# Kernel optimization log

Hardware: AMD Instinct MI355X
Metric: run time of the kernel (lower is better)

The kernel has to match this reference:

```python
import jax, jax.numpy as jnp
import numpy as np

B, S, H, V, T, NS, NB, NSW = 16, 200, 400, 25000, 8, 30, 3, 36


def setup_inputs() -> dict:
    key = jax.random.key(0)
    ks = jax.random.split(key, 12)
    return {
        "encoded_hidden": jax.random.normal(ks[0], (1, B, H), jnp.float32),
        "encoded_outputs": jax.random.normal(ks[1], (B, S, H), jnp.float32),
        "story": jax.random.randint(ks[2], (B, S), 0, V),
        "target_batches": jax.random.randint(ks[3], (B, NS, T), 0, V),
        "slot_dom_idx": jax.random.randint(ks[4], (NS,), 0, NSW),
        "slot_slot_idx": jax.random.randint(ks[5], (NS,), 0, NSW),
        "emb_W": jax.random.normal(ks[6], (V, H), jnp.float32) * 0.05,
        "slot_emb_W": jax.random.normal(ks[7], (NSW, H), jnp.float32) * 0.1,
        "gru_W_ih": jax.random.normal(ks[8], (3 * H, H), jnp.float32) * 0.05,
        "gru_W_hh": jax.random.normal(ks[9], (3 * H, H), jnp.float32) * 0.05,
        "gru_b_ih": jnp.zeros((3 * H,), jnp.float32),
        "gru_b_hh": jnp.zeros((3 * H,), jnp.float32),
        "W_ratio_w": jax.random.normal(ks[10], (1, 3 * H), jnp.float32) * 0.05,
        "W_ratio_b": jnp.zeros((1,), jnp.float32),
        "W_gate_w": jax.random.normal(ks[11], (NB, H), jnp.float32) * 0.05,
        "W_gate_b": jnp.zeros((NB,), jnp.float32),
    }


def reference(encoded_hidden, encoded_outputs, story, target_batches,
              slot_dom_idx, slot_slot_idx, emb_W, slot_emb_W,
              gru_W_ih, gru_W_hh, gru_b_ih, gru_b_hh,
              W_ratio_w, W_ratio_b, W_gate_w, W_gate_b):
    b, s, h = encoded_outputs.shape
    ns = slot_dom_idx.shape[0]
    v = emb_W.shape[0]
    t = target_batches.shape[2]
    bs = ns * b  # flattened slot*batch dim (parallel decode over slots)

    # slot embedding = domain_emb + slot_emb, broadcast over batch
    slot_emb = slot_emb_W[slot_dom_idx] + slot_emb_W[slot_slot_idx]        # [ns,h]
    dec_in0 = jnp.broadcast_to(slot_emb[:, None, :], (ns, b, h)).reshape(bs, h)
    h0 = jnp.tile(encoded_hidden[0], (ns, 1))                              # [bs,h]
    enc = jnp.tile(encoded_outputs, (ns, 1, 1))                            # [bs,s,h]
    pad_mask = jnp.tile(story == 0, (ns, 1))                               # [bs,s]
    story_rep = jnp.tile(story, (ns, 1))                                   # [bs,s]
    # teacher forcing targets, slot-major flatten: [bs, t]
    tf = jnp.transpose(target_batches, (1, 0, 2)).reshape(bs, t)
    rows = jnp.arange(bs)

    def gru_cell(x, hid):
        gx = x @ gru_W_ih.T + gru_b_ih
        gh = hid @ gru_W_hh.T + gru_b_hh
        r = jax.nn.sigmoid(gx[:, :h] + gh[:, :h])
        z = jax.nn.sigmoid(gx[:, h:2 * h] + gh[:, h:2 * h])
        n = jnp.tanh(gx[:, 2 * h:] + r * gh[:, 2 * h:])
        return (1.0 - z) * n + z * hid

    def step(carry, tgt_t):
        hid, x = carry
        hid = gru_cell(x, hid)                                             # [bs,h]
        scores = jnp.einsum('bh,bsh->bs', hid, enc)
        scores = jnp.where(pad_mask, -jnp.inf, scores)
        prob = jax.nn.softmax(scores, axis=1)                              # [bs,s]
        ctx = jnp.einsum('bs,bsh->bh', prob, enc)                          # [bs,h]
        p_vocab = jax.nn.softmax(hid @ emb_W.T, axis=1)                    # [bs,v]
        switch = jax.nn.sigmoid(
            jnp.concatenate([hid, ctx, x], axis=-1) @ W_ratio_w.T + W_ratio_b)  # [bs,1]
        p_ctx = jnp.zeros((bs, v), p_vocab.dtype).at[rows[:, None], story_rep].add(prob)
        final = (1.0 - switch) * p_ctx + switch * p_vocab                  # [bs,v]
        x_next = emb_W[tgt_t]                                              # teacher forcing
        return (hid, x_next), (final, ctx)

    (_, _), (finals, ctxs) = jax.lax.scan(step, (h0, dec_in0), tf.T)
    all_point = jnp.transpose(finals.reshape(t, ns, b, v), (1, 2, 0, 3))   # [ns,b,t,v]
    all_gate = (ctxs[0] @ W_gate_w.T + W_gate_b).reshape(ns, b, -1)        # [ns,b,nb_gate]
    return all_point, all_gate
```

## Files before the change

### kernel.cpp

```cpp
#include <hip/hip_runtime.h>
#include <math.h>

#define B_   16
#define S_   200
#define H_   400
#define V_   25000
#define T_   8
#define NS_  30
#define NB_  3
#define NSW_ 36
#define BS_  480

#define KP_  448
#define MP_  512
#define NP_  25088
#define NG_  1280
#define MA_  3840
#define NVT_ (NP_/128)
#define PSL_ 200

typedef unsigned short u16;
typedef __attribute__((ext_vector_type(4))) float f32x4;
typedef __attribute__((ext_vector_type(8))) short short8;

__device__ __forceinline__ u16 f2bf(float f) {
    unsigned u = __float_as_uint(f);
    u += 0x7FFFu + ((u >> 16) & 1u);
    return (u16)(u >> 16);
}
__device__ __forceinline__ float bf2f(u16 v) {
    return __uint_as_float(((unsigned)v) << 16);
}
__device__ __forceinline__ float wred_sum(float v) {
    v += __shfl_xor(v, 32); v += __shfl_xor(v, 16); v += __shfl_xor(v, 8);
    v += __shfl_xor(v, 4);  v += __shfl_xor(v, 2);  v += __shfl_xor(v, 1);
    return v;
}
__device__ __forceinline__ float wred_max(float v) {
    v = fmaxf(v, __shfl_xor(v, 32)); v = fmaxf(v, __shfl_xor(v, 16));
    v = fmaxf(v, __shfl_xor(v, 8));  v = fmaxf(v, __shfl_xor(v, 4));
    v = fmaxf(v, __shfl_xor(v, 2));  v = fmaxf(v, __shfl_xor(v, 1));
    return v;
}

__device__ __forceinline__ void gload_lds16(const void* g, void* l) {
    __builtin_amdgcn_global_load_lds(
        (const __attribute__((address_space(1))) void*)g,
        (__attribute__((address_space(3))) void*)l, 16, 0, 0);
}

#define MFMA_SETUP()                                                          \
    const int wid = tid >> 6, lane = tid & 63;                                \
    const int wr = wid >> 1, wc = wid & 1;                                    \
    f32x4 acc[4][4] = {};                                                     \
    const int sslot = lane & 7;                                               \
    const int srow8 = (lane >> 3) & 7;                                        \
    const int lcol = (sslot ^ srow8) * 8;                                     \
    const int lr = lane & 15, lg = lane >> 4, lx = lane & 7;                  \
    const int sA0 = (lg ^ lx) * 8, sA1 = ((4 + lg) ^ lx) * 8;

#define STAGE_TILE(k0_)                                                       \
    {                                                                         \
        _Pragma("unroll")                                                     \
        for (int is = 0; is < 4; ++is) {                                      \
            gload_lds16(Ag + (size_t)is * 8 * KP_ + (k0_),                    \
                        &As[(wid * 32 + is * 8) * 64]);                       \
            gload_lds16(Bg + (size_t)is * 8 * KP_ + (k0_),                    \
                        &Bs[(wid * 32 + is * 8) * 64]);                       \
        }                                                                     \
    }

#define COMPUTE_TILE()                                                        \
    {                                                                         \
        short8 af[4][2], bfr[4][2];                                           \
        _Pragma("unroll")                                                     \
        for (int i = 0; i < 4; ++i) {                                         \
            int ra = (wr * 64 + i * 16 + lr) * 64;                            \
            af[i][0] = *reinterpret_cast<const short8*>(&As[ra + sA0]);       \
            af[i][1] = *reinterpret_cast<const short8*>(&As[ra + sA1]);       \
            int rb = (wc * 64 + i * 16 + lr) * 64;                            \
            bfr[i][0] = *reinterpret_cast<const short8*>(&Bs[rb + sA0]);      \
            bfr[i][1] = *reinterpret_cast<const short8*>(&Bs[rb + sA1]);      \
        }                                                                     \
        _Pragma("unroll")                                                     \
        for (int h = 0; h < 2; ++h)                                           \
            _Pragma("unroll")                                                 \
            for (int i = 0; i < 4; ++i)                                       \
                _Pragma("unroll")                                             \
                for (int j = 0; j < 4; ++j)                                   \
                    acc[i][j] = __builtin_amdgcn_mfma_f32_16x16x32_bf16(      \
                        af[i][h], bfr[j][h], acc[i][j], 0, 0, 0);             \
    }

#define MFMA_KLOOP_SB()                                                       \
    _Pragma("unroll")                                                         \
    for (int kt = 0; kt < 7; ++kt) {                                          \
        STAGE_TILE(kt * 64);                                                  \
        __syncthreads();                                                      \
        COMPUTE_TILE();                                                       \
        __syncthreads();                                                      \
    }

__global__ void init_all(const float* __restrict__ eh, float* __restrict__ hid,
                         u16* __restrict__ Ab) {
    int i = blockIdx.x * blockDim.x + threadIdx.x;
    if (i >= MP_ * KP_) return;
    int row = i / KP_, d = i - row * KP_;
    u16 v = 0;
    if (row < BS_ && d < H_) {
        float h = eh[(row % B_) * H_ + d];
        hid[row * H_ + d] = h;
        v = f2bf(h);
    }
    Ab[i] = v;
}

__device__ __forceinline__ void conv_chunk(const float* __restrict__ src,
                                           u16* __restrict__ dst, int i, int rows) {
    int row = i / (KP_ / 8), c8 = (i - row * (KP_ / 8)) * 8;
    short8 o = {};
    if (row < rows && c8 < H_) {
        const float4* s = reinterpret_cast<const float4*>(src + (size_t)row * H_ + c8);
        float4 a = s[0], b = s[1];
        o[0] = (short)f2bf(a.x); o[1] = (short)f2bf(a.y);
        o[2] = (short)f2bf(a.z); o[3] = (short)f2bf(a.w);
        o[4] = (short)f2bf(b.x); o[5] = (short)f2bf(b.y);
        o[6] = (short)f2bf(b.z); o[7] = (short)f2bf(b.w);
    }
    *reinterpret_cast<short8*>(dst + (size_t)row * KP_ + c8) = o;
}

__global__ void conv_all(const float* __restrict__ embW, const float* __restrict__ Wih,
                         const float* __restrict__ Whh, u16* __restrict__ Bb,
                         u16* __restrict__ Wihb, u16* __restrict__ Whhb) {
    const int CB = NP_ * (KP_ / 8), CG = NG_ * (KP_ / 8);
    int i = blockIdx.x * blockDim.x + threadIdx.x;
    if (i < CB) conv_chunk(embW, Bb, i, V_);
    else if (i < CB + CG) conv_chunk(Wih, Wihb, i - CB, 3 * H_);
    else if (i < CB + 2 * CG) conv_chunk(Whh, Whhb, i - CB - CG, 3 * H_);
}

__global__ void xall_prep(const int* __restrict__ tb, const float* __restrict__ embW,
                          const float* __restrict__ sembW,
                          const int* __restrict__ dom, const int* __restrict__ sli,
                          float* __restrict__ x_all, u16* __restrict__ Xb_all) {
    int i = blockIdx.x * blockDim.x + threadIdx.x;
    if (i >= MA_ * (KP_ / 8)) return;
    int row = i / (KP_ / 8), c8 = (i - row * (KP_ / 8)) * 8;
    int t = row / BS_, r = row - t * BS_;
    int batch = r % B_, slot = r / B_;
    short8 o = {};
    if (c8 < H_) {
        float4 a, b;
        if (t == 0) {
            const float4* s0 = reinterpret_cast<const float4*>(sembW + dom[slot] * H_ + c8);
            const float4* s1 = reinterpret_cast<const float4*>(sembW + sli[slot] * H_ + c8);
            float4 x0 = s0[0], x1 = s0[1], y0 = s1[0], y1 = s1[1];
            a = make_float4(x0.x + y0.x, x0.y + y0.y, x0.z + y0.z, x0.w + y0.w);
            b = make_float4(x1.x + y1.x, x1.y + y1.y, x1.z + y1.z, x1.w + y1.w);
        } else {
            int tok = tb[(batch * NS_ + slot) * T_ + (t - 1)];
            const float4* s = reinterpret_cast<const float4*>(embW + (size_t)tok * H_ + c8);
            a = s[0]; b = s[1];
        }
        o[0] = (short)f2bf(a.x); o[1] = (short)f2bf(a.y);
        o[2] = (short)f2bf(a.z); o[3] = (short)f2bf(a.w);
        o[4] = (short)f2bf(b.x); o[5] = (short)f2bf(b.y);
        o[6] = (short)f2bf(b.z); o[7] = (short)f2bf(b.w);
        *reinterpret_cast<float4*>(x_all + (size_t)row * H_ + c8) = a;
        *reinterpret_cast<float4*>(x_all + (size_t)row * H_ + c8 + 4) = b;
    }
    *reinterpret_cast<short8*>(Xb_all + (size_t)row * KP_ + c8) = o;
}

__global__ __launch_bounds__(256)
void gemm_setup(const u16* __restrict__ Xb_all, const u16* __restrict__ Abuf,
                const u16* __restrict__ Wihb, const u16* __restrict__ Whhb,
                float* __restrict__ gx_all, float* __restrict__ gh) {
    __shared__ u16 As[128 * 64];
    __shared__ u16 Bs[128 * 64];
    const int tid = threadIdx.x;
    const bool mainp = blockIdx.y < (MA_ / 128);
    const int m0 = (mainp ? blockIdx.y : blockIdx.y - MA_ / 128) * 128;
    const int n0 = blockIdx.x * 128;
    const u16* A = mainp ? Xb_all : Abuf;
    const u16* Bw = mainp ? Wihb : Whhb;
    float* C = mainp ? gx_all : gh;
    const int Mlim = mainp ? MA_ : BS_;

    MFMA_SETUP();
    const u16* Ag = A + (size_t)(m0 + wid * 32 + (lane >> 3)) * KP_ + lcol;
    const u16* Bg = Bw + (size_t)(n0 + wid * 32 + (lane >> 3)) * KP_ + lcol;
    MFMA_KLOOP_SB();

    const int m_base = m0 + wr * 64 + lg * 4;
    const int n_base = n0 + wc * 64 + lr;
    #pragma unroll
    for (int i = 0; i < 4; ++i)
        #pragma unroll
        for (int r = 0; r < 4; ++r) {
            int m = m_base + i * 16 + r;
            if (m >= Mlim) continue;
            #pragma unroll
            for (int j = 0; j < 4; ++j) {
                int n = n_base + j * 16;
                if (n < 3 * H_) C[(size_t)m * 3 * H_ + n] = acc[i][j][r];
            }
        }
}

__global__ __launch_bounds__(256, 2)
void vocab_gh(const u16* __restrict__ A, const u16* __restrict__ Bb,
              const u16* __restrict__ Whhb, u16* __restrict__ pb,
              float* __restrict__ psum, float* __restrict__ gh) {
    __shared__ u16 As[256 * 64];
    __shared__ u16 Bs[128 * 64];
    __shared__ float sred[2][256];
    const int bid = blockIdx.x;
    const int tid = threadIdx.x;
    const int xcd = bid & 7, idx = bid >> 3;
    const int lin = (xcd < 4) ? (xcd * 52 + idx) : (208 + (xcd - 4) * 51 + idx);
    const int ntall = lin >> 1, mt = lin & 1;
    const bool isv = (ntall < NVT_);
    const int n0 = (isv ? ntall : ntall - NVT_) * 128;
    const int m0 = mt * 256;
    const u16* Bsrc = isv ? Bb : Whhb;

    const int wid = tid >> 6, lane = tid & 63;
    const int wr = wid >> 1, wc = wid & 1;
    f32x4 acc[8][4] = {};
    const int sslot = lane & 7;
    const int srow8 = (lane >> 3) & 7;
    const int lcol = (sslot ^ srow8) * 8;
    const int lr = lane & 15, lg = lane >> 4, lx = lane & 7;
    const int sA0 = (lg ^ lx) * 8, sA1 = ((4 + lg) ^ lx) * 8;

    const u16* Ag = A + (size_t)(m0 + wid * 64 + (lane >> 3)) * KP_ + lcol;
    const u16* Bg = Bsrc + (size_t)(n0 + wid * 32 + (lane >> 3)) * KP_ + lcol;

    for (int kt = 0; kt < 7; ++kt) {
        const int k0 = kt * 64;
        #pragma unroll
        for (int is = 0; is < 8; ++is)
            gload_lds16(Ag + (size_t)is * 8 * KP_ + k0, &As[(wid * 64 + is * 8) * 64]);
        #pragma unroll
        for (int is = 0; is < 4; ++is)
            gload_lds16(Bg + (size_t)is * 8 * KP_ + k0, &Bs[(wid * 32 + is * 8) * 64]);
        __syncthreads();
        #pragma unroll
        for (int h = 0; h < 2; ++h) {
            const int sA = h ? sA1 : sA0;
            short8 af[8], bf[4];
            #pragma unroll
            for (int i = 0; i < 8; ++i)
                af[i] = *reinterpret_cast<const short8*>(&As[(wr * 128 + i * 16 + lr) * 64 + sA]);
            #pragma unroll
            for (int j = 0; j < 4; ++j)
                bf[j] = *reinterpret_cast<const short8*>(&Bs[(wc * 64 + j * 16 + lr) * 64 + sA]);
            #pragma unroll
            for (int i = 0; i < 8; ++i)
                #pragma unroll
                for (int j = 0; j < 4; ++j)
                    acc[i][j] = __builtin_amdgcn_mfma_f32_16x16x32_bf16(
                        af[i], bf[j], acc[i][j], 0, 0, 0);
        }
        __syncthreads();
    }

    const int m_base = m0 + wr * 128 + lg * 4;
    const int n_base = n0 + wc * 64 + lr;
    if (isv) {
        #pragma unroll
        for (int i = 0; i < 8; ++i) {
            #pragma unroll
            for (int r = 0; r < 4; ++r) {
                int m = m_base + i * 16 + r;
                float js = 0.f;
                #pragma unroll
                for (int j = 0; j < 4; ++j) {
                    int n = n_base + j * 16;
                    float e = __expf(acc[i][j][r]);
                    if (m < BS_ && n < V_) {
                        pb[(size_t)m * V_ + n] = f2bf(e);
                        js += e;
                    }
                }
                js += __shfl_xor(js, 1);
                js += __shfl_xor(js, 2);
                js += __shfl_xor(js, 4);
                js += __shfl_xor(js, 8);
                if ((lane & 15) == 0) sred[wc][m - m0] = js;
            }
        }
        __syncthreads();
        {
            int m = m0 + tid;
            psum[(size_t)m * PSL_ + ntall] = sred[0][tid] + sred[1][tid];
        }
    } else {
        #pragma unroll
        for (int i = 0; i < 8; ++i)
            #pragma unroll
            for (int r = 0; r < 4; ++r) {
                int m = m_base + i * 16 + r;
                if (m >= BS_) continue;
                #pragma unroll
                for (int j = 0; j < 4; ++j) {
                    int n = n_base + j * 16;
                    if (n < 3 * H_) gh[(size_t)m * 3 * H_ + n] = acc[i][j][r];
                }
            }
    }
}

__global__ __launch_bounds__(256)
void attn_fin(const float* __restrict__ gx_all, const float* __restrict__ gh,
              const float* __restrict__ bih, const float* __restrict__ bhh,
              float* __restrict__ hid, u16* __restrict__ Ab,
              const float* __restrict__ x_all,
              const float* __restrict__ enc, const int* __restrict__ story,
              const float* __restrict__ Wr, const float* __restrict__ Wrb,
              const float* __restrict__ Wg, const float* __restrict__ Wgb,
              float* __restrict__ prob_cur, float* __restrict__ sw_cur,
              float* __restrict__ gate_out,
              float* __restrict__ out, const u16* __restrict__ pb,
              const float* __restrict__ psum, const float* __restrict__ sw_prev,
              const float* __restrict__ prob_prev, int t) {
    const int bid = blockIdx.x;
    const int lin = (bid & 7) * 120 + (bid >> 3);
    const int work = lin >> 1, kind = lin & 1;
    const int tid = threadIdx.x, w = tid >> 6, l = tid & 63;
    __shared__ __align__(16) float hs[H_];
    __shared__ __align__(16) float xs[H_];
    __shared__ __align__(16) float cs[H_];
    __shared__ float sc[S_];
    __shared__ float red[16];

    if (kind == 1) {
        if (t == 0) return;
        const int row = work, batch = row % B_;
        float rs = (tid < NVT_) ? psum[(size_t)row * PSL_ + tid] : 0.f;
        rs = wred_sum(rs);
        if (l == 0) red[w] = rs;
        __syncthreads();
        float denom = red[0] + red[1] + red[2] + red[3];
        float swv = sw_prev[row];
        float scl = swv / denom;
        const u16* ps = pb + (size_t)row * V_;
        float* p = out + ((size_t)row * T_ + (t - 1)) * V_;
        for (int v = tid * 8; v < V_; v += 256 * 8) {
            short8 in = *reinterpret_cast<const short8*>(ps + v);
            float4 o0, o1;
            o0.x = bf2f((u16)in[0]) * scl; o0.y = bf2f((u16)in[1]) * scl;
            o0.z = bf2f((u16)in[2]) * scl; o0.w = bf2f((u16)in[3]) * scl;
            o1.x = bf2f((u16)in[4]) * scl; o1.y = bf2f((u16)in[5]) * scl;
            o1.z = bf2f((u16)in[6]) * scl; o1.w = bf2f((u16)in[7]) * scl;
            *reinterpret_cast<float4*>(p + v) = o0;
            *reinterpret_cast<float4*>(p + v + 4) = o1;
        }
        __syncthreads();
        float om = 1.f - swv;
        for (int s = tid; s < S_; s += 256) {
            int tok = story[batch * S_ + s];
            atomicAdd(p + tok, om * prob_prev[(size_t)row * S_ + s]);
        }
        return;
    }

    const int batch = work / 30, slot = work - batch * 30;
    const int row = slot * B_ + batch;

    const float* gxr = gx_all + ((size_t)t * BS_ + row) * 3 * H_;
    const float* ghr = gh + (size_t)row * 3 * H_;
    const float* xr  = x_all + ((size_t)t * BS_ + row) * H_;
    for (int d = tid; d < H_; d += 256) {
        float r = 1.f / (1.f + expf(-(gxr[d] + bih[d] + ghr[d] + bhh[d])));
        float z = 1.f / (1.f + expf(-(gxr[H_ + d] + bih[H_ + d] + ghr[H_ + d] + bhh[H_ + d])));
        float n = tanhf(gxr[2 * H_ + d] + bih[2 * H_ + d] + r * (ghr[2 * H_ + d] + bhh[2 * H_ + d]));
        float h = (1.f - z) * n + z * hid[(size_t)row * H_ + d];
        hs[d] = h;
        hid[(size_t)row * H_ + d] = h;
        Ab[(size_t)row * KP_ + d] = f2bf(h);
        xs[d] = xr[d];
    }
    __syncthreads();

    const float* encb = enc + (size_t)batch * S_ * H_;
    {
        float4 hv1 = *reinterpret_cast<const float4*>(&hs[l * 4]);
        float4 hv2 = make_float4(0.f, 0.f, 0.f, 0.f);
        if (l < 36) hv2 = *reinterpret_cast<const float4*>(&hs[256 + l * 4]);
        for (int k = 0; k < 50; ++k) {
            int s = w * 50 + k;
            const float4* e = reinterpret_cast<const float4*>(encb + (size_t)s * H_);
            float4 ev = e[l];
            float part = ev.x * hv1.x + ev.y * hv1.y + ev.z * hv1.z + ev.w * hv1.w;
            if (l < 36) {
                float4 ev2 = e[64 + l];
                part += ev2.x * hv2.x + ev2.y * hv2.y + ev2.z * hv2.z + ev2.w * hv2.w;
            }
            part = wred_sum(part);
            if (l == 0)
                sc[s] = (story[batch * S_ + s] == 0) ? -1e30f : part;
        }
    }
    __syncthreads();

    float v = (tid < S_) ? sc[tid] : -1e30f;
    float wm = wred_max(v);
    if (l == 0) red[w] = wm;
    __syncthreads();
    float mx = fmaxf(fmaxf(red[0], red[1]), fmaxf(red[2], red[3]));
    float e = (tid < S_) ? __expf(v - mx) : 0.f;
    float wsum = wred_sum(e);
    if (l == 0) red[4 + w] = wsum;
    __syncthreads();
    float inv = 1.f / (red[4] + red[5] + red[6] + red[7]);
    if (tid < S_) {
        float pv = e * inv;
        sc[tid] = pv;
        prob_cur[(size_t)row * S_ + tid] = pv;
    }
    __syncthreads();

    for (int d = tid; d < H_; d += 256) {
        float a0 = 0.f, a1 = 0.f;
        for (int s = 0; s < S_; s += 2) {
            a0 += sc[s] * encb[(size_t)s * H_ + d];
            a1 += sc[s + 1] * encb[(size_t)(s + 1) * H_ + d];
        }
        cs[d] = a0 + a1;
    }
    __syncthreads();

    float part = 0.f;
    for (int i = tid; i < 3 * H_; i += 256) {
        float xv = (i < H_) ? hs[i] : (i < 2 * H_) ? cs[i - H_] : xs[i - 2 * H_];
        part += xv * Wr[i];
    }
    part = wred_sum(part);
    if (l == 0) red[8 + w] = part;
    __syncthreads();
    if (tid == 0)
        sw_cur[row] = 1.f / (1.f + expf(-(red[8] + red[9] + red[10] + red[11] + Wrb[0])));

    if (t == 0 && tid < NB_) {
        float acc = 0.f;
        for (int d = 0; d < H_; ++d) acc += cs[d] * Wg[tid * H_ + d];
        gate_out[(size_t)row * NB_ + tid] = acc + Wgb[tid];
    }
}

__global__ __launch_bounds__(256)
void scale_scatter(float* __restrict__ out, const u16* __restrict__ pb,
                   const float* __restrict__ psum, const float* __restrict__ sw,
                   const float* __restrict__ prob, const int* __restrict__ story) {
    const int row = blockIdx.x;
    const int tid = threadIdx.x, w = tid >> 6, l = tid & 63;
    __shared__ float red[4];
    float rs = (tid < NVT_) ? psum[(size_t)row * PSL_ + tid] : 0.f;
    rs = wred_sum(rs);
    if (l == 0) red[w] = rs;
    __syncthreads();
    float denom = red[0] + red[1] + red[2] + red[3];
    float swv = sw[row];
    float scl = swv / denom;
    const u16* ps = pb + (size_t)row * V_;
    float* p = out + ((size_t)row * T_ + (T_ - 1)) * V_;
    for (int v = tid * 8; v < V_; v += 256 * 8) {
        short8 in = *reinterpret_cast<const short8*>(ps + v);
        float4 o0, o1;
        o0.x = bf2f((u16)in[0]) * scl; o0.y = bf2f((u16)in[1]) * scl;
        o0.z = bf2f((u16)in[2]) * scl; o0.w = bf2f((u16)in[3]) * scl;
        o1.x = bf2f((u16)in[4]) * scl; o1.y = bf2f((u16)in[5]) * scl;
        o1.z = bf2f((u16)in[6]) * scl; o1.w = bf2f((u16)in[7]) * scl;
        *reinterpret_cast<float4*>(p + v) = o0;
        *reinterpret_cast<float4*>(p + v + 4) = o1;
    }
    __syncthreads();
    const int batch = row % B_;
    float om = 1.f - swv;
    for (int s = tid; s < S_; s += 256) {
        int tok = story[batch * S_ + s];
        atomicAdd(p + tok, om * prob[(size_t)row * S_ + s]);
    }
}

extern "C" void kernel_launch(void* const* d_in, const int* in_sizes, int n_in,
                              void* d_out, int out_size, void* d_ws, size_t ws_size,
                              hipStream_t stream) {
    const float* eh    = (const float*)d_in[0];
    const float* enc   = (const float*)d_in[1];
    const int*   story = (const int*)d_in[2];
    const int*   tb    = (const int*)d_in[3];
    const int*   dom   = (const int*)d_in[4];
    const int*   sli   = (const int*)d_in[5];
    const float* embW  = (const float*)d_in[6];
    const float* sembW = (const float*)d_in[7];
    const float* Wih   = (const float*)d_in[8];
    const float* Whh   = (const float*)d_in[9];
    const float* bih   = (const float*)d_in[10];
    const float* bhh   = (const float*)d_in[11];
    const float* Wr    = (const float*)d_in[12];
    const float* Wrb   = (const float*)d_in[13];
    const float* Wg    = (const float*)d_in[14];
    const float* Wgb   = (const float*)d_in[15];

    float* out = (float*)d_out;
    float* ws  = (float*)d_ws;

    float* gx_all = ws;
    float* gh     = gx_all + (size_t)MA_ * 3 * H_;
    float* hid    = gh + (size_t)BS_ * 3 * H_;
    float* x_all  = hid + (size_t)BS_ * H_;
    float* prob2  = x_all + (size_t)MA_ * H_;
    float* sw2    = prob2 + 2 * BS_ * S_;
    float* psum   = sw2 + 2 * BS_;
    u16* Ab     = (u16*)(psum + (size_t)MP_ * PSL_);
    u16* Xb_all = Ab + (size_t)MP_ * KP_;
    u16* Wihb   = Xb_all + (size_t)MA_ * KP_;
    u16* Whhb   = Wihb + (size_t)NG_ * KP_;
    u16* Bb     = Whhb + (size_t)NG_ * KP_;
    u16* pb     = Bb + (size_t)NP_ * KP_;
    size_t need = (size_t)((char*)(pb + (size_t)BS_ * V_) - (char*)ws);
    if (ws_size < need) return;

    float* gate_out = out + (size_t)NS_ * B_ * T_ * V_;

    init_all<<<(MP_ * KP_ + 255) / 256, 256, 0, stream>>>(eh, hid, Ab);
    {
        int tot = (NP_ + 2 * NG_) * (KP_ / 8);
        conv_all<<<(tot + 255) / 256, 256, 0, stream>>>(embW, Wih, Whh, Bb, Wihb, Whhb);
    }
    xall_prep<<<(MA_ * (KP_ / 8) + 255) / 256, 256, 0, stream>>>(tb, embW, sembW, dom, sli,
                                                                 x_all, Xb_all);
    gemm_setup<<<dim3(NG_ / 128, MA_ / 128 + MP_ / 128), 256, 0, stream>>>(
        Xb_all, Ab, Wihb, Whhb, gx_all, gh);

    for (int t = 0; t < T_; ++t) {
        const int cur = t & 1, prev = cur ^ 1;
        attn_fin<<<960, 256, 0, stream>>>(gx_all, gh, bih, bhh, hid, Ab, x_all,
                                          enc, story, Wr, Wrb, Wg, Wgb,
                                          prob2 + cur * BS_ * S_, sw2 + cur * BS_,
                                          gate_out, out, pb, psum,
                                          sw2 + prev * BS_, prob2 + prev * BS_ * S_, t);
        vocab_gh<<<412, 256, 0, stream>>>(Ab, Bb, Whhb, pb, psum, gh);
    }
    {
        const int last = (T_ - 1) & 1;
        scale_scatter<<<BS_, 256, 0, stream>>>(out, pb, psum, sw2 + last * BS_,
                                               prob2 + last * BS_ * S_, story);
    }
}
```

Baseline: 777.9 us.

## Double-buffer B tiles in vocab GEMM and merge prep kernels into one launch

The vocab_gh K-loop now double-buffers the B (weight) tile in shared memory. It prefetches the next K-slice while computing the current one, uses an explicit vmcnt wait instead of waiting for all loads, and replaces __syncthreads with raw s_barrier. The three setup kernels (init, weight conversion, x_all prep) are fused into one prep_all launch to save launch overhead. The gemm_setup macros are inlined with no functional change. The risks are extra LDS use, which may lower occupancy, and the hand-written waitcnt count, which must match the number of outstanding loads exactly or the kernel will read incomplete data.

```diff
diff --git a/kernel.cpp b/kernel.cpp
--- a/kernel.cpp
+++ b/kernel.cpp
@@ -8,7 +8,6 @@
 #define T_   8
 #define NS_  30
 #define NB_  3
-#define NSW_ 36
 #define BS_  480
 
 #define KP_  448
@@ -42,7 +41,6 @@
     v = fmaxf(v, __shfl_xor(v, 2));  v = fmaxf(v, __shfl_xor(v, 1));
     return v;
 }
-
 __device__ __forceinline__ void gload_lds16(const void* g, void* l) {
     __builtin_amdgcn_global_load_lds(
         (const __attribute__((address_space(1))) void*)g,
@@ -53,124 +51,76 @@
     const int wid = tid >> 6, lane = tid & 63;                                \
     const int wr = wid >> 1, wc = wid & 1;                                    \
     f32x4 acc[4][4] = {};                                                     \
-    const int sslot = lane & 7;                                               \
-    const int srow8 = (lane >> 3) & 7;                                        \
-    const int lcol = (sslot ^ srow8) * 8;                                     \
+    const int lcol = ((lane & 7) ^ ((lane >> 3) & 7)) * 8;                    \
     const int lr = lane & 15, lg = lane >> 4, lx = lane & 7;                  \
     const int sA0 = (lg ^ lx) * 8, sA1 = ((4 + lg) ^ lx) * 8;
 
-#define STAGE_TILE(k0_)                                                       \
-    {                                                                         \
-        _Pragma("unroll")                                                     \
-        for (int is = 0; is < 4; ++is) {                                      \
-            gload_lds16(Ag + (size_t)is * 8 * KP_ + (k0_),                    \
-                        &As[(wid * 32 + is * 8) * 64]);                       \
-            gload_lds16(Bg + (size_t)is * 8 * KP_ + (k0_),                    \
-                        &Bs[(wid * 32 + is * 8) * 64]);                       \
-        }                                                                     \
-    }
-
-#define COMPUTE_TILE()                                                        \
-    {                                                                         \
-        short8 af[4][2], bfr[4][2];                                           \
-        _Pragma("unroll")                                                     \
-        for (int i = 0; i < 4; ++i) {                                         \
-            int ra = (wr * 64 + i * 16 + lr) * 64;                            \
-            af[i][0] = *reinterpret_cast<const short8*>(&As[ra + sA0]);       \
-            af[i][1] = *reinterpret_cast<const short8*>(&As[ra + sA1]);       \
-            int rb = (wc * 64 + i * 16 + lr) * 64;                            \
-            bfr[i][0] = *reinterpret_cast<const short8*>(&Bs[rb + sA0]);      \
-            bfr[i][1] = *reinterpret_cast<const short8*>(&Bs[rb + sA1]);      \
-        }                                                                     \
-        _Pragma("unroll")                                                     \
-        for (int h = 0; h < 2; ++h)                                           \
-            _Pragma("unroll")                                                 \
-            for (int i = 0; i < 4; ++i)                                       \
-                _Pragma("unroll")                                             \
-                for (int j = 0; j < 4; ++j)                                   \
-                    acc[i][j] = __builtin_amdgcn_mfma_f32_16x16x32_bf16(      \
-                        af[i][h], bfr[j][h], acc[i][j], 0, 0, 0);             \
-    }
-
-#define MFMA_KLOOP_SB()                                                       \
-    _Pragma("unroll")                                                         \
-    for (int kt = 0; kt < 7; ++kt) {                                          \
-        STAGE_TILE(kt * 64);                                                  \
-        __syncthreads();                                                      \
-        COMPUTE_TILE();                                                       \
-        __syncthreads();                                                      \
-    }
-
-__global__ void init_all(const float* __restrict__ eh, float* __restrict__ hid,
-                         u16* __restrict__ Ab) {
-    int i = blockIdx.x * blockDim.x + threadIdx.x;
-    if (i >= MP_ * KP_) return;
-    int row = i / KP_, d = i - row * KP_;
-    u16 v = 0;
-    if (row < BS_ && d < H_) {
-        float h = eh[(row % B_) * H_ + d];
-        hid[row * H_ + d] = h;
-        v = f2bf(h);
-    }
-    Ab[i] = v;
-}
-
-__device__ __forceinline__ void conv_chunk(const float* __restrict__ src,
-                                           u16* __restrict__ dst, int i, int rows) {
-    int row = i / (KP_ / 8), c8 = (i - row * (KP_ / 8)) * 8;
-    short8 o = {};
-    if (row < rows && c8 < H_) {
-        const float4* s = reinterpret_cast<const float4*>(src + (size_t)row * H_ + c8);
-        float4 a = s[0], b = s[1];
-        o[0] = (short)f2bf(a.x); o[1] = (short)f2bf(a.y);
-        o[2] = (short)f2bf(a.z); o[3] = (short)f2bf(a.w);
-        o[4] = (short)f2bf(b.x); o[5] = (short)f2bf(b.y);
-        o[6] = (short)f2bf(b.z); o[7] = (short)f2bf(b.w);
-    }
-    *reinterpret_cast<short8*>(dst + (size_t)row * KP_ + c8) = o;
-}
-
-__global__ void conv_all(const float* __restrict__ embW, const float* __restrict__ Wih,
-                         const float* __restrict__ Whh, u16* __restrict__ Bb,
-                         u16* __restrict__ Wihb, u16* __restrict__ Whhb) {
+__global__ void prep_all(const float* __restrict__ eh, const float* __restrict__ embW,
+                         const float* __restrict__ Wih, const float* __restrict__ Whh,
+                         const float* __restrict__ sembW, const int* __restrict__ tb,
+                         const int* __restrict__ dom, const int* __restrict__ sli,
+                         float* __restrict__ hid, u16* __restrict__ Ab,
+                         u16* __restrict__ Bb, u16* __restrict__ Wihb, u16* __restrict__ Whhb,
+                         float* __restrict__ x_all, u16* __restrict__ Xb_all) {
+    const int R0 = MP_ * KP_;
     const int CB = NP_ * (KP_ / 8), CG = NG_ * (KP_ / 8);
-    int i = blockIdx.x * blockDim.x + threadIdx.x;
-    if (i < CB) conv_chunk(embW, Bb, i, V_);
-    else if (i < CB + CG) conv_chunk(Wih, Wihb, i - CB, 3 * H_);
-    else if (i < CB + 2 * CG) conv_chunk(Whh, Whhb, i - CB - CG, 3 * H_);
-}
-
-__global__ void xall_prep(const int* __restrict__ tb, const float* __restrict__ embW,
-                          const float* __restrict__ sembW,
-                          const int* __restrict__ dom, const int* __restrict__ sli,
-                          float* __restrict__ x_all, u16* __restrict__ Xb_all) {
-    int i = blockIdx.x * blockDim.x + threadIdx.x;
-    if (i >= MA_ * (KP_ / 8)) return;
-    int row = i / (KP_ / 8), c8 = (i - row * (KP_ / 8)) * 8;
-    int t = row / BS_, r = row - t * BS_;
-    int batch = r % B_, slot = r / B_;
-    short8 o = {};
-    if (c8 < H_) {
-        float4 a, b;
-        if (t == 0) {
-            const float4* s0 = reinterpret_cast<const float4*>(sembW + dom[slot] * H_ + c8);
-            const float4* s1 = reinterpret_cast<const float4*>(sembW + sli[slot] * H_ + c8);
-            float4 x0 = s0[0], x1 = s0[1], y0 = s1[0], y1 = s1[1];
-            a = make_float4(x0.x + y0.x, x0.y + y0.y, x0.z + y0.z, x0.w + y0.w);
-            b = make_float4(x1.x + y1.x, x1.y + y1.y, x1.z + y1.z, x1.w + y1.w);
-        } else {
-            int tok = tb[(batch * NS_ + slot) * T_ + (t - 1)];
-            const float4* s = reinterpret_cast<const float4*>(embW + (size_t)tok * H_ + c8);
-            a = s[0]; b = s[1];
-        }
-        o[0] = (short)f2bf(a.x); o[1] = (short)f2bf(a.y);
-        o[2] = (short)f2bf(a.z); o[3] = (short)f2bf(a.w);
-        o[4] = (short)f2bf(b.x); o[5] = (short)f2bf(b.y);
-        o[6] = (short)f2bf(b.z); o[7] = (short)f2bf(b.w);
-        *reinterpret_cast<float4*>(x_all + (size_t)row * H_ + c8) = a;
-        *reinterpret_cast<float4*>(x_all + (size_t)row * H_ + c8 + 4) = b;
-    }
-    *reinterpret_cast<short8*>(Xb_all + (size_t)row * KP_ + c8) = o;
+    const int R1 = R0 + CB + 2 * CG;
+    const int R2 = R1 + MA_ * (KP_ / 8);
+    int i = blockIdx.x * 256 + threadIdx.x;
+    if (i < R0) {
+        int row = i / KP_, d = i - row * KP_;
+        u16 v = 0;
+        if (row < BS_ && d < H_) {
+            float h = eh[(row % B_) * H_ + d];
+            hid[row * H_ + d] = h;
+            v = f2bf(h);
+        }
+        Ab[i] = v;
+    } else if (i < R1) {
+        int j = i - R0;
+        const float* src; u16* dst; int rows;
+        if (j < CB) { src = embW; dst = Bb; rows = V_; }
+        else if (j < CB + CG) { src = Wih; dst = Wihb; rows = 3 * H_; j -= CB; }
+        else { src = Whh; dst = Whhb; rows = 3 * H_; j -= CB + CG; }
+        int row = j / (KP_ / 8), c8 = (j - row * (KP_ / 8)) * 8;
+        short8 o = {};
+        if (row < rows && c8 < H_) {
+            const float4* s = reinterpret_cast<const float4*>(src + (size_t)row * H_ + c8);
+            float4 a = s[0], b = s[1];
+            o[0] = (short)f2bf(a.x); o[1] = (short)f2bf(a.y);
+            o[2] = (short)f2bf(a.z); o[3] = (short)f2bf(a.w);
+            o[4] = (short)f2bf(b.x); o[5] = (short)f2bf(b.y);
+            o[6] = (short)f2bf(b.z); o[7] = (short)f2bf(b.w);
+        }
+        *reinterpret_cast<short8*>(dst + (size_t)row * KP_ + c8) = o;
+    } else if (i < R2) {
+        int j = i - R1;
+        int row = j / (KP_ / 8), c8 = (j - row * (KP_ / 8)) * 8;
+        int t = row / BS_, r = row - t * BS_;
+        int batch = r % B_, slot = r / B_;
+        short8 o = {};
+        if (c8 < H_) {
+            float4 a, b;
+            if (t == 0) {
+                const float4* s0 = reinterpret_cast<const float4*>(sembW + dom[slot] * H_ + c8);
+                const float4* s1 = reinterpret_cast<const float4*>(sembW + sli[slot] * H_ + c8);
+                float4 x0 = s0[0], x1 = s0[1], y0 = s1[0], y1 = s1[1];
+                a = make_float4(x0.x + y0.x, x0.y + y0.y, x0.z + y0.z, x0.w + y0.w);
+                b = make_float4(x1.x + y1.x, x1.y + y1.y, x1.z + y1.z, x1.w + y1.w);
+            } else {
+                int tok = tb[(batch * NS_ + slot) * T_ + (t - 1)];
+                const float4* s = reinterpret_cast<const float4*>(embW + (size_t)tok * H_ + c8);
+                a = s[0]; b = s[1];
+            }
+            o[0] = (short)f2bf(a.x); o[1] = (short)f2bf(a.y);
+            o[2] = (short)f2bf(a.z); o[3] = (short)f2bf(a.w);
+            o[4] = (short)f2bf(b.x); o[5] = (short)f2bf(b.y);
+            o[6] = (short)f2bf(b.z); o[7] = (short)f2bf(b.w);
+            *reinterpret_cast<float4*>(x_all + (size_t)row * H_ + c8) = a;
+            *reinterpret_cast<float4*>(x_all + (size_t)row * H_ + c8 + 4) = b;
+        }
+        *reinterpret_cast<short8*>(Xb_all + (size_t)row * KP_ + c8) = o;
+    }
 }
 
 __global__ __launch_bounds__(256)
@@ -191,8 +141,35 @@
     MFMA_SETUP();
     const u16* Ag = A + (size_t)(m0 + wid * 32 + (lane >> 3)) * KP_ + lcol;
     const u16* Bg = Bw + (size_t)(n0 + wid * 32 + (lane >> 3)) * KP_ + lcol;
-    MFMA_KLOOP_SB();
-
+
+    for (int kt = 0; kt < 7; ++kt) {
+        const int k0 = kt * 64;
+        #pragma unroll
+        for (int is = 0; is < 4; ++is) {
+            gload_lds16(Ag + (size_t)is * 8 * KP_ + k0, &As[(wid * 32 + is * 8) * 64]);
+            gload_lds16(Bg + (size_t)is * 8 * KP_ + k0, &Bs[(wid * 32 + is * 8) * 64]);
+        }
+        __syncthreads();
+        short8 af[4][2], bfr[4][2];
+        #pragma unroll
+        for (int i = 0; i < 4; ++i) {
+            int ra = (wr * 64 + i * 16 + lr) * 64;
+            af[i][0] = *reinterpret_cast<const short8*>(&As[ra + sA0]);
+            af[i][1] = *reinterpret_cast<const short8*>(&As[ra + sA1]);
+            int rb = (wc * 64 + i * 16 + lr) * 64;
+            bfr[i][0] = *reinterpret_cast<const short8*>(&Bs[rb + sA0]);
+            bfr[i][1] = *reinterpret_cast<const short8*>(&Bs[rb + sA1]);
+        }
+        #pragma unroll
+        for (int h = 0; h < 2; ++h)
+            #pragma unroll
+            for (int i = 0; i < 4; ++i)
+                #pragma unroll
+                for (int j = 0; j < 4; ++j)
+                    acc[i][j] = __builtin_amdgcn_mfma_f32_16x16x32_bf16(
+                        af[i][h], bfr[j][h], acc[i][j], 0, 0, 0);
+        __syncthreads();
+    }
     const int m_base = m0 + wr * 64 + lg * 4;
     const int n_base = n0 + wc * 64 + lr;
     #pragma unroll
@@ -214,7 +191,7 @@
               const u16* __restrict__ Whhb, u16* __restrict__ pb,
               float* __restrict__ psum, float* __restrict__ gh) {
     __shared__ u16 As[256 * 64];
-    __shared__ u16 Bs[128 * 64];
+    __shared__ u16 Bs[2][128 * 64];
     __shared__ float sred[2][256];
     const int bid = blockIdx.x;
     const int tid = threadIdx.x;
@@ -229,24 +206,33 @@
     const int wid = tid >> 6, lane = tid & 63;
     const int wr = wid >> 1, wc = wid & 1;
     f32x4 acc[8][4] = {};
-    const int sslot = lane & 7;
-    const int srow8 = (lane >> 3) & 7;
-    const int lcol = (sslot ^ srow8) * 8;
+    const int lcol = ((lane & 7) ^ ((lane >> 3) & 7)) * 8;
     const int lr = lane & 15, lg = lane >> 4, lx = lane & 7;
     const int sA0 = (lg ^ lx) * 8, sA1 = ((4 + lg) ^ lx) * 8;
-
     const u16* Ag = A + (size_t)(m0 + wid * 64 + (lane >> 3)) * KP_ + lcol;
     const u16* Bg = Bsrc + (size_t)(n0 + wid * 32 + (lane >> 3)) * KP_ + lcol;
 
+    #pragma unroll
+    for (int is = 0; is < 4; ++is)
+        gload_lds16(Bg + (size_t)is * 8 * KP_, &Bs[0][(wid * 32 + is * 8) * 64]);
+
     for (int kt = 0; kt < 7; ++kt) {
-        const int k0 = kt * 64;
+        const int k0 = kt * 64, cur = kt & 1;
         #pragma unroll
         for (int is = 0; is < 8; ++is)
             gload_lds16(Ag + (size_t)is * 8 * KP_ + k0, &As[(wid * 64 + is * 8) * 64]);
-        #pragma unroll
-        for (int is = 0; is < 4; ++is)
-            gload_lds16(Bg + (size_t)is * 8 * KP_ + k0, &Bs[(wid * 32 + is * 8) * 64]);
-        __syncthreads();
+        if (kt < 6) {
+            #pragma unroll
+            for (int is = 0; is < 4; ++is)
+                gload_lds16(Bg + (size_t)is * 8 * KP_ + k0 + 64,
+                            &Bs[cur ^ 1][(wid * 32 + is * 8) * 64]);
+            asm volatile("s_waitcnt vmcnt(4)" ::: "memory");
+        } else {
+            asm volatile("s_waitcnt vmcnt(0)" ::: "memory");
+        }
+        __builtin_amdgcn_sched_barrier(0);
+        __builtin_amdgcn_s_barrier();
+        const u16* Bsl = Bs[cur];
         #pragma unroll
         for (int h = 0; h < 2; ++h) {
             const int sA = h ? sA1 : sA0;
@@ -256,7 +242,7 @@
                 af[i] = *reinterpret_cast<const short8*>(&As[(wr * 128 + i * 16 + lr) * 64 + sA]);
             #pragma unroll
             for (int j = 0; j < 4; ++j)
-                bf[j] = *reinterpret_cast<const short8*>(&Bs[(wc * 64 + j * 16 + lr) * 64 + sA]);
+                bf[j] = *reinterpret_cast<const short8*>(&Bsl[(wc * 64 + j * 16 + lr) * 64 + sA]);
             #pragma unroll
             for (int i = 0; i < 8; ++i)
                 #pragma unroll
@@ -264,7 +250,7 @@
                     acc[i][j] = __builtin_amdgcn_mfma_f32_16x16x32_bf16(
                         af[i], bf[j], acc[i][j], 0, 0, 0);
         }
-        __syncthreads();
+        __builtin_amdgcn_s_barrier();
     }
 
     const int m_base = m0 + wr * 128 + lg * 4;
@@ -527,13 +513,11 @@
 
     float* gate_out = out + (size_t)NS_ * B_ * T_ * V_;
 
-    init_all<<<(MP_ * KP_ + 255) / 256, 256, 0, stream>>>(eh, hid, Ab);
     {
-        int tot = (NP_ + 2 * NG_) * (KP_ / 8);
-        conv_all<<<(tot + 255) / 256, 256, 0, stream>>>(embW, Wih, Whh, Bb, Wihb, Whhb);
-    }
-    xall_prep<<<(MA_ * (KP_ / 8) + 255) / 256, 256, 0, stream>>>(tb, embW, sembW, dom, sli,
-                                                                 x_all, Xb_all);
+        const int R2 = MP_ * KP_ + (NP_ + 2 * NG_) * (KP_ / 8) + MA_ * (KP_ / 8);
+        prep_all<<<(R2 + 255) / 256, 256, 0, stream>>>(eh, embW, Wih, Whh, sembW, tb, dom, sli,
+                                                       hid, Ab, Bb, Wihb, Whhb, x_all, Xb_all);
+    }
     gemm_setup<<<dim3(NG_ / 128, MA_ / 128 + MP_ / 128), 256, 0, stream>>>(
         Xb_all, Ab, Wihb, Whhb, gx_all, gh);
 
```

New measurement: 769.2 us. About the same (-1.1%).
